# Optimization experiments

Hardware: AMD Instinct MI355X
Metric: run time of the kernel (lower is better)

## Reference

```python
import jax, jax.numpy as jnp
import numpy as np

DIM = 4194304
EPS = 1e-24


def setup_inputs() -> dict:
    key = jax.random.key(0)
    ks = jax.random.split(key, 17)
    dim = DIM
    s = 0.3  # weight scale ~ kaiming for small fan-in
    inp = {
        "gradient": jax.random.normal(ks[0], (dim,), jnp.float32),
        "x_prev": jax.random.normal(ks[1], (dim,), jnp.float32),
        "x_curr": jax.random.normal(ks[2], (dim,), jnp.float32),
        "loss_curr": jax.random.uniform(ks[3], (1,), jnp.float32),
        "loss_prev": jax.random.uniform(ks[4], (1,), jnp.float32),
        "Wc1": s * jax.random.normal(ks[5], (10, 3), jnp.float32),
        "Wc2": s * jax.random.normal(ks[6], (10, 10), jnp.float32),
        "Wc3": s * jax.random.normal(ks[7], (10, 10), jnp.float32),
        "Wc4": s * jax.random.normal(ks[8], (10, 10), jnp.float32),
        "Wc5": s * jax.random.normal(ks[9], (10, 10), jnp.float32),
        "Wc6": s * jax.random.normal(ks[10], (10, 10), jnp.float32),
        "Wc7": s * jax.random.normal(ks[11], (1, 10), jnp.float32),
        "Wl1": s * jax.random.normal(ks[12], (8, 4), jnp.float32),
        "Wl2": s * jax.random.normal(ks[13], (8, 8), jnp.float32),
        "Wl3": s * jax.random.normal(ks[14], (8, 8), jnp.float32),
        "Wl4": s * jax.random.normal(ks[15], (8, 8), jnp.float32),
        "Wl5": s * jax.random.normal(ks[16], (1, 8), jnp.float32),
    }
    return inp


def reference(gradient, x_prev, x_curr, loss_curr, loss_prev,
              Wc1, Wc2, Wc3, Wc4, Wc5, Wc6, Wc7,
              Wl1, Wl2, Wl3, Wl4, Wl5):
    relu = jax.nn.relu

    g_norm = jnp.linalg.norm(gradient)
    g = jnp.where(g_norm > EPS, gradient / g_norm, gradient)

    momentum = x_curr - x_prev
    m_norm = jnp.linalg.norm(momentum)
    m = jnp.where(m_norm > EPS, momentum / m_norm, momentum)

    # coefficients MLP on log(1 + scalar features); losses are detached in torch
    feats = jnp.log1p(jnp.stack([
        g_norm,
        m_norm,
        jax.lax.stop_gradient(loss_curr[0]),
        jax.lax.stop_gradient(loss_prev[0]),
    ]))  # [4]
    h = relu(Wl1 @ feats)
    h = relu(Wl2 @ h)
    h = relu(Wl3 @ h)
    h = Wl4 @ h
    step_size = Wl5 @ h  # [1]

    # direction network: 1x1 convs over the parameter dimension -> channel matmuls
    x = jnp.stack([g, m, g * m], axis=0)  # [3, dim]
    d = Wc1 @ x          # conv1 (no activation)
    d = Wc2 @ d          # conv2
    d = relu(d)
    d = relu(Wc3 @ d)
    d = relu(Wc4 @ d)
    d = relu(Wc5 @ d)
    d = Wc6 @ d          # conv6 (no activation)
    d = Wc7 @ d          # conv7 -> [1, dim]
    direction = d.reshape(-1)  # [dim]

    return x_curr - step_size * direction
```

## Files before the change

### kernel.cpp

```cpp
#include <hip/hip_runtime.h>
#include <math.h>
#include <stdint.h>

#define DIM 4194304
#define RBLOCKS 1024
#define RTHREADS 256
#define FBLOCKS 2048
#define FTHREADS 256
#define TOTTH (FBLOCKS * FTHREADS)
#define PASSES (DIM / TOTTH)
#define EPSF 1e-24f
#define SCALE 256.0f

#define WS_PART 0
#define WS_W21 2048
#define WS_W3 2176
#define WS_W4 2304
#define WS_W5 2432
#define WS_W67 2560

typedef uint32_t u32;
typedef __fp16 fp16x2 __attribute__((ext_vector_type(2)));
typedef __fp16 half8 __attribute__((ext_vector_type(8)));
typedef float f32x4 __attribute__((ext_vector_type(4)));
typedef uint32_t u32x2 __attribute__((ext_vector_type(2)));
typedef uint32_t u32x4 __attribute__((ext_vector_type(4)));

__device__ __forceinline__ u32 pack2u(float a, float b) {
    fp16x2 r = __builtin_amdgcn_cvt_pkrtz(a, b);
    return __builtin_bit_cast(u32, r);
}
__device__ __forceinline__ u32 pkmul(u32 a, u32 b) {
    fp16x2 r = __builtin_bit_cast(fp16x2, a) * __builtin_bit_cast(fp16x2, b);
    return __builtin_bit_cast(u32, r);
}

__device__ __forceinline__ f32x4 mfma32(half8 a, half8 b, f32x4 c) {
    return __builtin_amdgcn_mfma_f32_16x16x32_f16(a, b, c, 0, 0, 0);
}
__device__ __forceinline__ half8 relucvt8(f32x4 a) {
    fp16x2 z2 = {(__fp16)0.f, (__fp16)0.f};
    fp16x2 c0 = __builtin_amdgcn_cvt_pkrtz(a[0], a[1]);
    fp16x2 c1 = __builtin_amdgcn_cvt_pkrtz(a[2], a[3]);
    c0 = __builtin_elementwise_max(c0, z2);
    c1 = __builtin_elementwise_max(c1, z2);
    u32x4 r = {__builtin_bit_cast(u32, c0), __builtin_bit_cast(u32, c1), 0u, 0u};
    return __builtin_bit_cast(half8, r);
}

__global__ __launch_bounds__(RTHREADS) void k_reduce(
    const float* __restrict__ grad, const float* __restrict__ xp, const float* __restrict__ xc,
    const float* __restrict__ Wc1, const float* __restrict__ Wc2, const float* __restrict__ Wc3,
    const float* __restrict__ Wc4, const float* __restrict__ Wc5, const float* __restrict__ Wc6,
    const float* __restrict__ Wc7, float* __restrict__ ws) {
    if (blockIdx.x == 0) {
        u32* wsu = (u32*)ws;
        int t = threadIdx.x;
        if (t < 128) {
            int lane = t >> 1, d = t & 1;
            int m = lane & 15, gg = lane >> 4;
            int k0 = 4 * gg + 2 * d;
            float a0 = 0.f, a1 = 0.f;
            if (m < 10 && k0 < 3) {
                for (int j = 0; j < 10; ++j) a0 += Wc2[m * 10 + j] * Wc1[j * 3 + k0];
                if (k0 == 2) a0 *= (1.f / SCALE);
            }
            if (m < 10 && k0 + 1 < 3) {
                for (int j = 0; j < 10; ++j) a1 += Wc2[m * 10 + j] * Wc1[j * 3 + k0 + 1];
                if (k0 + 1 == 2) a1 *= (1.f / SCALE);
            }
            wsu[WS_W21 + t] = pack2u(a0, a1);
            float v0, v1;
            v0 = (m < 10 && k0 < 10) ? Wc3[m * 10 + k0] : 0.f;
            v1 = (m < 10 && k0 + 1 < 10) ? Wc3[m * 10 + k0 + 1] : 0.f;
            wsu[WS_W3 + t] = pack2u(v0, v1);
            v0 = (m < 10 && k0 < 10) ? Wc4[m * 10 + k0] : 0.f;
            v1 = (m < 10 && k0 + 1 < 10) ? Wc4[m * 10 + k0 + 1] : 0.f;
            wsu[WS_W4 + t] = pack2u(v0, v1);
            v0 = (m < 10 && k0 < 10) ? Wc5[m * 10 + k0] : 0.f;
            v1 = (m < 10 && k0 + 1 < 10) ? Wc5[m * 10 + k0 + 1] : 0.f;
            wsu[WS_W5 + t] = pack2u(v0, v1);
        }
        if (t >= 128 && t < 144) {
            int j = t - 128;
            float w = 0.f;
            if (j < 10)
                for (int k = 0; k < 10; ++k) w += Wc7[k] * Wc6[k * 10 + j];
            ws[WS_W67 + j] = w;
        }
    }
    const float4* g4 = reinterpret_cast<const float4*>(grad);
    const float4* p4 = reinterpret_cast<const float4*>(xp);
    const float4* c4 = reinterpret_cast<const float4*>(xc);
    int tid = blockIdx.x * RTHREADS + threadIdx.x;
    float sg = 0.f, sm = 0.f;
    constexpr int STRIDE = RBLOCKS * RTHREADS;
#pragma unroll
    for (int it = 0; it < (DIM / 4) / STRIDE; ++it) {
        int i = tid + it * STRIDE;
        float4 gv = g4[i];
        float4 pv = p4[i];
        float4 cv = c4[i];
        sg += gv.x * gv.x + gv.y * gv.y + gv.z * gv.z + gv.w * gv.w;
        float mx = cv.x - pv.x, my = cv.y - pv.y, mz = cv.z - pv.z, mw = cv.w - pv.w;
        sm += mx * mx + my * my + mz * mz + mw * mw;
    }
#pragma unroll
    for (int off = 32; off > 0; off >>= 1) {
        sg += __shfl_down(sg, off);
        sm += __shfl_down(sm, off);
    }
    __shared__ float wg[4], wm[4];
    int wave = threadIdx.x >> 6;
    if ((threadIdx.x & 63) == 0) {
        wg[wave] = sg;
        wm[wave] = sm;
    }
    __syncthreads();
    if (threadIdx.x == 0) {
        ws[WS_PART + 2 * blockIdx.x]     = wg[0] + wg[1] + wg[2] + wg[3];
        ws[WS_PART + 2 * blockIdx.x + 1] = wm[0] + wm[1] + wm[2] + wm[3];
    }
}

__global__ __launch_bounds__(FTHREADS, 4) void k_fused(
    const float* __restrict__ grad, const float* __restrict__ xp, const float* __restrict__ xc,
    const float* __restrict__ loss_curr, const float* __restrict__ loss_prev,
    const float* __restrict__ Wl1, const float* __restrict__ Wl2, const float* __restrict__ Wl3,
    const float* __restrict__ Wl4, const float* __restrict__ Wl5,
    const float* __restrict__ ws, float* __restrict__ out) {
    __shared__ float sc[3];
    __shared__ float red[8];
    const int tid = threadIdx.x;
    const int lane = tid & 63;

    const int ebase = (blockIdx.x * (FTHREADS / 64) + (tid >> 6)) * 64 + lane;
    float gvv = grad[ebase], pvv = xp[ebase], cvv = xc[ebase];

    {
        float fg = 0.f, fm = 0.f;
        for (int i = tid; i < RBLOCKS; i += FTHREADS) {
            fg += ws[WS_PART + 2 * i];
            fm += ws[WS_PART + 2 * i + 1];
        }
#pragma unroll
        for (int off = 32; off > 0; off >>= 1) {
            fg += __shfl_down(fg, off);
            fm += __shfl_down(fm, off);
        }
        int wv = tid >> 6;
        if ((tid & 63) == 0) {
            red[wv] = fg;
            red[4 + wv] = fm;
        }
        __syncthreads();
        if (tid < 64) {
            float g2 = red[0] + red[1] + red[2] + red[3];
            float m2 = red[4] + red[5] + red[6] + red[7];
            float g_norm = sqrtf(g2), m_norm = sqrtf(m2);
            float g_inv = (g_norm > EPSF) ? 1.f / g_norm : 1.f;
            float m_inv = (m_norm > EPSF) ? 1.f / m_norm : 1.f;
            float feats[4] = {log1pf(g_norm), log1pf(m_norm), log1pf(loss_curr[0]),
                              log1pf(loss_prev[0])};
            float h1[8], h2_[8], h3[8], h4[8];
#pragma unroll
            for (int o = 0; o < 8; ++o) {
                float acc = 0.f;
#pragma unroll
                for (int i = 0; i < 4; ++i) acc += Wl1[o * 4 + i] * feats[i];
                h1[o] = fmaxf(acc, 0.f);
            }
#pragma unroll
            for (int o = 0; o < 8; ++o) {
                float acc = 0.f;
#pragma unroll
                for (int i = 0; i < 8; ++i) acc += Wl2[o * 8 + i] * h1[i];
                h2_[o] = fmaxf(acc, 0.f);
            }
#pragma unroll
            for (int o = 0; o < 8; ++o) {
                float acc = 0.f;
#pragma unroll
                for (int i = 0; i < 8; ++i) acc += Wl3[o * 8 + i] * h2_[i];
                h3[o] = fmaxf(acc, 0.f);
            }
#pragma unroll
            for (int o = 0; o < 8; ++o) {
                float acc = 0.f;
#pragma unroll
                for (int i = 0; i < 8; ++i) acc += Wl4[o * 8 + i] * h3[i];
                h4[o] = acc;
            }
            float step = 0.f;
#pragma unroll
            for (int i = 0; i < 8; ++i) step += Wl5[i] * h4[i];
            if (tid == 0) {
                sc[0] = g_inv * SCALE;
                sc[1] = m_inv * SCALE;
                sc[2] = step * (1.f / SCALE);
            }
        }
        __syncthreads();
    }
    const float gs = sc[0], ms = sc[1], step_eff = sc[2];

    const u32* wsu = (const u32*)ws;
    const int n = lane & 15, g = lane >> 4;
#define LOADFRAG(NAME, OFS)                                                    \
    half8 NAME;                                                                \
    {                                                                          \
        u32x2 lo = ((const u32x2*)(wsu + (OFS)))[lane];                        \
        u32x4 fr = {lo[0], lo[1], 0u, 0u};                                     \
        NAME = __builtin_bit_cast(half8, fr);                                  \
    }
    LOADFRAG(w21f, WS_W21)
    LOADFRAG(w3f, WS_W3)
    LOADFRAG(w4f, WS_W4)
    LOADFRAG(w5f, WS_W5)
#undef LOADFRAG
    half8 w67f;
    {
        const float* w67p = ws + WS_W67;
        u32x4 fr = {pack2u(w67p[4 * g], w67p[4 * g + 1]),
                    pack2u(w67p[4 * g + 2], w67p[4 * g + 3]), 0u, 0u};
        w67f = __builtin_bit_cast(half8, fr);
    }
    const f32x4 zf = {0.f, 0.f, 0.f, 0.f};
    const int idxv[4] = {n << 2, (n + 16) << 2, (n + 32) << 2, (n + 48) << 2};

    int e = ebase;
#pragma unroll
    for (int p = 0; p < PASSES; ++p) {
        int en = (p + 1 < PASSES) ? (e + TOTTH) : 0;
        float gvn = grad[en], pvn = xp[en], cvn = xc[en];

        float Gf = gvv * gs;
        float Mf = (cvv - pvv) * ms;
        u32 pk0 = pack2u(Gf, Mf);

        float dhalf0, dhalf1;
#pragma unroll
        for (int st = 0; st < 2; ++st) {
            u32 b0[2];
#pragma unroll
            for (int t = 0; t < 2; ++t)
                b0[t] = (u32)__builtin_amdgcn_ds_bpermute(idxv[2 * st + t], (int)pk0);
            f32x4 acc[2];
#pragma unroll
            for (int t = 0; t < 2; ++t) {
                u32 b1 = pkmul(b0[t], (b0[t] >> 16) | (b0[t] << 16));
                u32x4 bb = {b0[t], b1, 0u, 0u};
                acc[t] = mfma32(w21f, __builtin_bit_cast(half8, bb), zf);
            }
#pragma unroll
            for (int t = 0; t < 2; ++t) acc[t] = mfma32(w3f, relucvt8(acc[t]), zf);
#pragma unroll
            for (int t = 0; t < 2; ++t) acc[t] = mfma32(w4f, relucvt8(acc[t]), zf);
#pragma unroll
            for (int t = 0; t < 2; ++t) acc[t] = mfma32(w5f, relucvt8(acc[t]), zf);
#pragma unroll
            for (int t = 0; t < 2; ++t) acc[t] = mfma32(w67f, relucvt8(acc[t]), zf);
            float dsel = ((g & 1) == 0) ? acc[0][0] : acc[1][0];
            if (st == 0)
                dhalf0 = dsel;
            else
                dhalf1 = dsel;
        }
        float dsel = (g < 2) ? dhalf0 : dhalf1;
        out[e] = fmaf(-step_eff, dsel, cvv);

        e = (p + 1 < PASSES) ? en : e;
        gvv = gvn;
        pvv = pvn;
        cvv = cvn;
    }
}

extern "C" void kernel_launch(void* const* d_in, const int* in_sizes, int n_in,
                              void* d_out, int out_size, void* d_ws, size_t ws_size,
                              hipStream_t stream) {
    const float* grad      = (const float*)d_in[0];
    const float* xp        = (const float*)d_in[1];
    const float* xc        = (const float*)d_in[2];
    const float* loss_curr = (const float*)d_in[3];
    const float* loss_prev = (const float*)d_in[4];
    const float* Wc1 = (const float*)d_in[5];
    const float* Wc2 = (const float*)d_in[6];
    const float* Wc3 = (const float*)d_in[7];
    const float* Wc4 = (const float*)d_in[8];
    const float* Wc5 = (const float*)d_in[9];
    const float* Wc6 = (const float*)d_in[10];
    const float* Wc7 = (const float*)d_in[11];
    const float* Wl1 = (const float*)d_in[12];
    const float* Wl2 = (const float*)d_in[13];
    const float* Wl3 = (const float*)d_in[14];
    const float* Wl4 = (const float*)d_in[15];
    const float* Wl5 = (const float*)d_in[16];

    float* ws  = (float*)d_ws;
    float* out = (float*)d_out;

    k_reduce<<<RBLOCKS, RTHREADS, 0, stream>>>(grad, xp, xc, Wc1, Wc2, Wc3, Wc4, Wc5, Wc6,
                                               Wc7, ws);
    k_fused<<<FBLOCKS, FTHREADS, 0, stream>>>(grad, xp, xc, loss_curr, loss_prev, Wl1, Wl2,
                                              Wl3, Wl4, Wl5, ws, out);
}
```

Measured before the change: 41.12 us.

## Move final norm reduction and MLP into last-block of reduce kernel

The final reduction of per-block partial norms and the scalar coefficient MLP move out of every block of the fused kernel into the last-arriving block of the reduce kernel, chosen through an atomic ticket reset by a memset. The fused kernel then only reads three precomputed scalars, which drops a redundant per-block reduction and a __syncthreads, and its occupancy hint rises to 8. The g*m product is now computed in fp32 and broadcast with a second bpermute instead of an fp16 packed multiply. This adds a memset launch, a threadfence and atomic in the reduce kernel, plus extra LDS permute traffic.

```diff
diff --git a/kernel.cpp b/kernel.cpp
--- a/kernel.cpp
+++ b/kernel.cpp
@@ -18,6 +18,8 @@
 #define WS_W4 2304
 #define WS_W5 2432
 #define WS_W67 2560
+#define WS_SC 2576
+#define WS_TICKET 2592
 
 typedef uint32_t u32;
 typedef __fp16 fp16x2 __attribute__((ext_vector_type(2)));
@@ -28,10 +30,6 @@
 
 __device__ __forceinline__ u32 pack2u(float a, float b) {
     fp16x2 r = __builtin_amdgcn_cvt_pkrtz(a, b);
-    return __builtin_bit_cast(u32, r);
-}
-__device__ __forceinline__ u32 pkmul(u32 a, u32 b) {
-    fp16x2 r = __builtin_bit_cast(fp16x2, a) * __builtin_bit_cast(fp16x2, b);
     return __builtin_bit_cast(u32, r);
 }
 
@@ -50,12 +48,16 @@
 
 __global__ __launch_bounds__(RTHREADS) void k_reduce(
     const float* __restrict__ grad, const float* __restrict__ xp, const float* __restrict__ xc,
+    const float* __restrict__ loss_curr, const float* __restrict__ loss_prev,
     const float* __restrict__ Wc1, const float* __restrict__ Wc2, const float* __restrict__ Wc3,
     const float* __restrict__ Wc4, const float* __restrict__ Wc5, const float* __restrict__ Wc6,
-    const float* __restrict__ Wc7, float* __restrict__ ws) {
+    const float* __restrict__ Wc7, const float* __restrict__ Wl1, const float* __restrict__ Wl2,
+    const float* __restrict__ Wl3, const float* __restrict__ Wl4, const float* __restrict__ Wl5,
+    float* __restrict__ ws) {
+    const int tid = threadIdx.x;
     if (blockIdx.x == 0) {
         u32* wsu = (u32*)ws;
-        int t = threadIdx.x;
+        int t = tid;
         if (t < 128) {
             int lane = t >> 1, d = t & 1;
             int m = lane & 15, gg = lane >> 4;
@@ -89,57 +91,53 @@
             ws[WS_W67 + j] = w;
         }
     }
-    const float4* g4 = reinterpret_cast<const float4*>(grad);
-    const float4* p4 = reinterpret_cast<const float4*>(xp);
-    const float4* c4 = reinterpret_cast<const float4*>(xc);
-    int tid = blockIdx.x * RTHREADS + threadIdx.x;
-    float sg = 0.f, sm = 0.f;
-    constexpr int STRIDE = RBLOCKS * RTHREADS;
-#pragma unroll
-    for (int it = 0; it < (DIM / 4) / STRIDE; ++it) {
-        int i = tid + it * STRIDE;
-        float4 gv = g4[i];
-        float4 pv = p4[i];
-        float4 cv = c4[i];
-        sg += gv.x * gv.x + gv.y * gv.y + gv.z * gv.z + gv.w * gv.w;
-        float mx = cv.x - pv.x, my = cv.y - pv.y, mz = cv.z - pv.z, mw = cv.w - pv.w;
-        sm += mx * mx + my * my + mz * mz + mw * mw;
-    }
-#pragma unroll
-    for (int off = 32; off > 0; off >>= 1) {
-        sg += __shfl_down(sg, off);
-        sm += __shfl_down(sm, off);
-    }
-    __shared__ float wg[4], wm[4];
-    int wave = threadIdx.x >> 6;
-    if ((threadIdx.x & 63) == 0) {
-        wg[wave] = sg;
-        wm[wave] = sm;
-    }
+    {
+        const float4* g4 = reinterpret_cast<const float4*>(grad);
+        const float4* p4 = reinterpret_cast<const float4*>(xp);
+        const float4* c4 = reinterpret_cast<const float4*>(xc);
+        int gt = blockIdx.x * RTHREADS + tid;
+        float sg = 0.f, sm = 0.f;
+        constexpr int STRIDE = RBLOCKS * RTHREADS;
+#pragma unroll
+        for (int it = 0; it < (DIM / 4) / STRIDE; ++it) {
+            int i = gt + it * STRIDE;
+            float4 gv = g4[i];
+            float4 pv = p4[i];
+            float4 cv = c4[i];
+            sg += gv.x * gv.x + gv.y * gv.y + gv.z * gv.z + gv.w * gv.w;
+            float mx = cv.x - pv.x, my = cv.y - pv.y, mz = cv.z - pv.z, mw = cv.w - pv.w;
+            sm += mx * mx + my * my + mz * mz + mw * mw;
+        }
+#pragma unroll
+        for (int off = 32; off > 0; off >>= 1) {
+            sg += __shfl_down(sg, off);
+            sm += __shfl_down(sm, off);
+        }
+        __shared__ float wg[4], wm[4];
+        int wave = tid >> 6;
+        if ((tid & 63) == 0) {
+            wg[wave] = sg;
+            wm[wave] = sm;
+        }
+        __syncthreads();
+        if (tid == 0) {
+            ws[WS_PART + 2 * blockIdx.x]     = wg[0] + wg[1] + wg[2] + wg[3];
+            ws[WS_PART + 2 * blockIdx.x + 1] = wm[0] + wm[1] + wm[2] + wm[3];
+        }
+    }
+    __shared__ unsigned int is_last;
+    __threadfence();
     __syncthreads();
-    if (threadIdx.x == 0) {
-        ws[WS_PART + 2 * blockIdx.x]     = wg[0] + wg[1] + wg[2] + wg[3];
-        ws[WS_PART + 2 * blockIdx.x + 1] = wm[0] + wm[1] + wm[2] + wm[3];
-    }
-}
-
-__global__ __launch_bounds__(FTHREADS, 4) void k_fused(
-    const float* __restrict__ grad, const float* __restrict__ xp, const float* __restrict__ xc,
-    const float* __restrict__ loss_curr, const float* __restrict__ loss_prev,
-    const float* __restrict__ Wl1, const float* __restrict__ Wl2, const float* __restrict__ Wl3,
-    const float* __restrict__ Wl4, const float* __restrict__ Wl5,
-    const float* __restrict__ ws, float* __restrict__ out) {
-    __shared__ float sc[3];
-    __shared__ float red[8];
-    const int tid = threadIdx.x;
-    const int lane = tid & 63;
-
-    const int ebase = (blockIdx.x * (FTHREADS / 64) + (tid >> 6)) * 64 + lane;
-    float gvv = grad[ebase], pvv = xp[ebase], cvv = xc[ebase];
-
-    {
+    if (tid == 0) {
+        unsigned int t = atomicAdd((unsigned int*)((u32*)ws + WS_TICKET), 1u);
+        is_last = (t == (unsigned int)(RBLOCKS - 1)) ? 1u : 0u;
+    }
+    __syncthreads();
+    if (is_last) {
+        __threadfence();
+        __shared__ float red[8];
         float fg = 0.f, fm = 0.f;
-        for (int i = tid; i < RBLOCKS; i += FTHREADS) {
+        for (int i = tid; i < RBLOCKS; i += RTHREADS) {
             fg += ws[WS_PART + 2 * i];
             fm += ws[WS_PART + 2 * i + 1];
         }
@@ -154,7 +152,7 @@
             red[4 + wv] = fm;
         }
         __syncthreads();
-        if (tid < 64) {
+        if (tid == 0) {
             float g2 = red[0] + red[1] + red[2] + red[3];
             float m2 = red[4] + red[5] + red[6] + red[7];
             float g_norm = sqrtf(g2), m_norm = sqrtf(m2);
@@ -194,15 +192,21 @@
             float step = 0.f;
 #pragma unroll
             for (int i = 0; i < 8; ++i) step += Wl5[i] * h4[i];
-            if (tid == 0) {
-                sc[0] = g_inv * SCALE;
-                sc[1] = m_inv * SCALE;
-                sc[2] = step * (1.f / SCALE);
-            }
-        }
-        __syncthreads();
-    }
-    const float gs = sc[0], ms = sc[1], step_eff = sc[2];
+            ws[WS_SC + 0] = g_inv * SCALE;
+            ws[WS_SC + 1] = m_inv * SCALE;
+            ws[WS_SC + 2] = step * (1.f / SCALE);
+        }
+    }
+}
+
+__global__ __launch_bounds__(FTHREADS, 8) void k_fused(const float* __restrict__ grad,
+                                                       const float* __restrict__ xp,
+                                                       const float* __restrict__ xc,
+                                                       const float* __restrict__ ws,
+                                                       float* __restrict__ out) {
+    const int tid = threadIdx.x;
+    const int lane = tid & 63;
+    const float gs = ws[WS_SC + 0], ms = ws[WS_SC + 1], step_eff = ws[WS_SC + 2];
 
     const u32* wsu = (const u32*)ws;
     const int n = lane & 15, g = lane >> 4;
@@ -226,9 +230,10 @@
         w67f = __builtin_bit_cast(half8, fr);
     }
     const f32x4 zf = {0.f, 0.f, 0.f, 0.f};
-    const int idxv[4] = {n << 2, (n + 16) << 2, (n + 32) << 2, (n + 48) << 2};
-
+
+    int ebase = (blockIdx.x * (FTHREADS / 64) + (tid >> 6)) * 64 + lane;
     int e = ebase;
+    float gvv = grad[e], pvv = xp[e], cvv = xc[e];
 #pragma unroll
     for (int p = 0; p < PASSES; ++p) {
         int en = (p + 1 < PASSES) ? (e + TOTTH) : 0;
@@ -236,20 +241,23 @@
 
         float Gf = gvv * gs;
         float Mf = (cvv - pvv) * ms;
-        u32 pk0 = pack2u(Gf, Mf);
+        float GMf = Gf * Mf;
+        u32 pk0 = pack2u(Gf, Mf), pk1 = pack2u(GMf, 0.f);
 
         float dhalf0, dhalf1;
 #pragma unroll
         for (int st = 0; st < 2; ++st) {
-            u32 b0[2];
-#pragma unroll
-            for (int t = 0; t < 2; ++t)
-                b0[t] = (u32)__builtin_amdgcn_ds_bpermute(idxv[2 * st + t], (int)pk0);
+            u32 b0[2], b1[2];
+#pragma unroll
+            for (int t = 0; t < 2; ++t) {
+                int idx = (n + 16 * (2 * st + t)) << 2;
+                b0[t] = (u32)__builtin_amdgcn_ds_bpermute(idx, (int)pk0);
+                b1[t] = (u32)__builtin_amdgcn_ds_bpermute(idx, (int)pk1);
+            }
             f32x4 acc[2];
 #pragma unroll
             for (int t = 0; t < 2; ++t) {
-                u32 b1 = pkmul(b0[t], (b0[t] >> 16) | (b0[t] << 16));
-                u32x4 bb = {b0[t], b1, 0u, 0u};
+                u32x4 bb = {b0[t], b1[t], 0u, 0u};
                 acc[t] = mfma32(w21f, __builtin_bit_cast(half8, bb), zf);
             }
 #pragma unroll
@@ -300,8 +308,9 @@
     float* ws  = (float*)d_ws;
     float* out = (float*)d_out;
 
-    k_reduce<<<RBLOCKS, RTHREADS, 0, stream>>>(grad, xp, xc, Wc1, Wc2, Wc3, Wc4, Wc5, Wc6,
-                                               Wc7, ws);
-    k_fused<<<FBLOCKS, FTHREADS, 0, stream>>>(grad, xp, xc, loss_curr, loss_prev, Wl1, Wl2,
-                                              Wl3, Wl4, Wl5, ws, out);
-}
+    hipMemsetAsync((uint32_t*)ws + WS_TICKET, 0, sizeof(uint32_t), stream);
+    k_reduce<<<RBLOCKS, RTHREADS, 0, stream>>>(grad, xp, xc, loss_curr, loss_prev, Wc1, Wc2,
+                                               Wc3, Wc4, Wc5, Wc6, Wc7, Wl1, Wl2, Wl3, Wl4,
+                                               Wl5, ws);
+    k_fused<<<FBLOCKS, FTHREADS, 0, stream>>>(grad, xp, xc, ws, out);
+}
```

Measured after the change: 147.2 us. 3.58x slower.
